# Performance work log

Measured on AMD Instinct MI355X. Metric: run time of the kernel, lower is better.

## Reference

```python
import jax, jax.numpy as jnp
import numpy as np

IN_SIZE = 1024
CLASSES = 7
N = 50000
LN_EPS = 1e-5


def _chain(x, w, b, g, beta):
    # Linear -> (Dropout=identity at eval) -> LayerNorm -> GELU(exact erf)
    h = x @ w.T + b
    mu = jnp.mean(h, axis=-1, keepdims=True)
    var = jnp.var(h, axis=-1, keepdims=True)
    h = (h - mu) / jnp.sqrt(var + LN_EPS) * g + beta
    return jax.nn.gelu(h, approximate=False)


def setup_inputs() -> dict:
    key = jax.random.key(0)
    ks = jax.random.split(key, 16)
    d = IN_SIZE
    std = 1.0 / np.sqrt(d)
    inp = {
        "features": jax.random.normal(ks[0], (N, d), jnp.float32),
        "c": jax.random.normal(ks[1], (N, CLASSES), jnp.float32),
        "key_w": jax.random.uniform(ks[2], (d, d), jnp.float32, -std, std),
        "key_b": jax.random.uniform(ks[3], (d,), jnp.float32, -std, std),
        "key_g": jnp.ones((d,), jnp.float32),
        "key_beta": jnp.zeros((d,), jnp.float32),
        "query_w": jax.random.uniform(ks[4], (d, d), jnp.float32, -std, std),
        "query_b": jax.random.uniform(ks[5], (d,), jnp.float32, -std, std),
        "query_g": jnp.ones((d,), jnp.float32),
        "query_beta": jnp.zeros((d,), jnp.float32),
        "value_w": jax.random.uniform(ks[6], (d, d), jnp.float32, -std, std),
        "value_b": jax.random.uniform(ks[7], (d,), jnp.float32, -std, std),
        "value_g": jnp.ones((d,), jnp.float32),
        "value_beta": jnp.zeros((d,), jnp.float32),
        "head_w": jax.random.uniform(ks[8], (CLASSES, CLASSES, d), jnp.float32, -1.0 / np.sqrt(CLASSES * d), 1.0 / np.sqrt(CLASSES * d)),
        "head_b": jax.random.uniform(ks[9], (CLASSES,), jnp.float32, -1.0 / np.sqrt(CLASSES * d), 1.0 / np.sqrt(CLASSES * d)),
    }
    return inp


def reference(features, c, key_w, key_b, key_g, key_beta,
              query_w, query_b, query_g, query_beta,
              value_w, value_b, value_g, value_beta,
              head_w, head_b):
    K = _chain(features, key_w, key_b, key_g, key_beta)          # [N, d]
    V = _chain(K, value_w, value_b, value_g, value_beta)         # [N, d]
    Q = _chain(K, query_w, query_b, query_g, query_beta)         # [N, d]
    # critical (top-scoring) instance per class
    top_idx = jnp.argmax(c, axis=0)                              # [classes]
    m_feats = K[top_idx]                                         # [classes, d]
    q_max = _chain(m_feats, query_w, query_b, query_g, query_beta)  # [classes, d]
    A = Q @ q_max.T                                              # [N, classes]
    A = jax.nn.softmax(A / jnp.sqrt(jnp.float32(Q.shape[1])), axis=0)
    B = A.T @ V                                                  # [classes, d]
    # Conv1d(classes, classes, kernel_size=d) on [1, classes, d] -> full contraction
    C = jnp.einsum('ik,oik->o', B, head_w) + head_b              # [classes]
    C = C.reshape(1, -1)
    return (C, A, B.reshape(1, CLASSES, -1))
```

## Files before the change

### kernel.cpp

```cpp
#include <hip/hip_runtime.h>


typedef unsigned short u16;
typedef __attribute__((ext_vector_type(8))) short          bf16x8;
typedef __attribute__((ext_vector_type(8))) unsigned short u16x8;
typedef __attribute__((ext_vector_type(4))) unsigned short u16x4;
typedef __attribute__((ext_vector_type(4))) float          f32x4;

#define DDIM  1024
#define NROWS 50000
#define MP    50176
#define NCLS  7
#define MPD4  12544

__device__ __forceinline__ u16 f2bf(float f) {
  unsigned u = __float_as_uint(f);
  u = (u + 0x7FFFu + ((u >> 16) & 1u)) >> 16;
  return (u16)u;
}
__device__ __forceinline__ float bf2f(u16 h) {
  return __uint_as_float(((unsigned)h) << 16);
}
__device__ __forceinline__ float gelu(float x) {
  return 0.5f * x * (1.0f + erff(x * 0.70710678118654752f));
}

__device__ __forceinline__ void load16_lds(const u16* g, u16* l) {
  __builtin_amdgcn_global_load_lds(
      (const __attribute__((address_space(1))) unsigned int*)(const void*)g,
      (__attribute__((address_space(3))) unsigned int*)(void*)l, 16, 0, 0);
}

#define MFMA_(a, b, c) __builtin_amdgcn_mfma_f32_16x16x32_bf16(a, b, c, 0, 0, 0)

__global__ __launch_bounds__(256) void k_convert(const float* __restrict__ src,
                                                 u16* __restrict__ dst,
                                                 int rows_total, int rows_valid) {
  const size_t total = (size_t)rows_total * DDIM / 8;
  const size_t stride = (size_t)gridDim.x * blockDim.x;
  for (size_t i = (size_t)blockIdx.x * blockDim.x + threadIdx.x; i < total; i += stride) {
    const size_t e = i * 8;
    const int row = (int)(e >> 10);
    u16x8 o = {0, 0, 0, 0, 0, 0, 0, 0};
    if (row < rows_valid) {
      const float4* p = (const float4*)(src + e);
      float4 f0 = p[0], f1 = p[1];
      o[0] = f2bf(f0.x); o[1] = f2bf(f0.y); o[2] = f2bf(f0.z); o[3] = f2bf(f0.w);
      o[4] = f2bf(f1.x); o[5] = f2bf(f1.y); o[6] = f2bf(f1.z); o[7] = f2bf(f1.w);
    }
    *(u16x8*)(dst + e) = o;
  }
}

__global__ __launch_bounds__(256) void k_convw(const float* __restrict__ kw,
                                               const float* __restrict__ vw,
                                               const float* __restrict__ qw,
                                               u16* __restrict__ Wk,
                                               u16* __restrict__ Wvq) {
  const int w = blockIdx.x >> 7;
  const int b = blockIdx.x & 127;
  const float* src = (w == 0) ? kw : (w == 1) ? vw : qw;
  u16* dst = (w == 0) ? Wk : (Wvq + (size_t)(w - 1) * DDIM * DDIM);
  for (int i = b * 256 + threadIdx.x; i < DDIM * DDIM / 8; i += 128 * 256) {
    const float4* p = (const float4*)(src + (size_t)i * 8);
    float4 f0 = p[0], f1 = p[1];
    u16x8 o;
    o[0] = f2bf(f0.x); o[1] = f2bf(f0.y); o[2] = f2bf(f0.z); o[3] = f2bf(f0.w);
    o[4] = f2bf(f1.x); o[5] = f2bf(f1.y); o[6] = f2bf(f1.z); o[7] = f2bf(f1.w);
    *(u16x8*)(dst + (size_t)i * 8) = o;
  }
}

__global__ __launch_bounds__(512, 2) void k_gemm256(const u16* __restrict__ A,
                                                    const u16* __restrict__ Bw,
                                                    u16* __restrict__ C,
                                                    int lnn, int ldc) {
  extern __shared__ __align__(16) u16 smem[];
  u16* Abase = smem;
  u16* Bbase = smem + 49152;
  const int tid  = threadIdx.x;
  const int lane = tid & 63;
  const int wid  = tid >> 6;
  const int wr = wid >> 2;
  const int wc = wid & 3;
  const int bh = wc >> 1;
  const int bl = (wc & 1) * 64;
  const int fr = lane & 15;
  const int T  = lane >> 4;
  const int cpx = gridDim.x >> 3;
  const int v  = (blockIdx.x & 7) * cpx + (blockIdx.x >> 3);
  const int m0 = (v >> lnn) * 256;
  const int n0 = (v & ((1 << lnn) - 1)) * 256;

  f32x4 acc[8][4] = {};

#define STAGE_A(KT, BB) do {                                                   \
    _Pragma("unroll") for (int h_ = 0; h_ < 2; ++h_)                           \
      _Pragma("unroll") for (int l_ = 0; l_ < 2; ++l_) {                       \
        const int s_ = l_ * 512 + tid;                                         \
        const int r_ = s_ >> 3;                                                \
        const int c_ = (s_ & 7) ^ (r_ & 7);                                    \
        load16_lds(A + (size_t)(m0 + h_ * 128 + r_) * DDIM + (KT) * 64 + c_ * 8, \
                   Abase + (BB) * 16384 + h_ * 8192 + s_ * 8);                 \
      } } while (0)

#define STAGE_B(KT) do {                                                       \
    _Pragma("unroll") for (int h_ = 0; h_ < 2; ++h_)                           \
      _Pragma("unroll") for (int l_ = 0; l_ < 2; ++l_) {                       \
        const int s_ = l_ * 512 + tid;                                         \
        const int r_ = s_ >> 3;                                                \
        const int c_ = (s_ & 7) ^ (r_ & 7);                                    \
        load16_lds(Bw + (size_t)(n0 + h_ * 128 + r_) * DDIM + (KT) * 64 + c_ * 8, \
                   Bbase + h_ * 8192 + s_ * 8);                                \
      } } while (0)

#define PHASE_A(p) do {                                                        \
    bf16x8 afr[4];                                                             \
    _Pragma("unroll") for (int ks = 0; ks < 2; ++ks)                           \
      _Pragma("unroll") for (int ii = 0; ii < 2; ++ii) {                       \
        const int R = ((p) * 2 + ii) * 16 + fr;                                \
        afr[ks * 2 + ii] = *(const bf16x8*)&Ap[R * 64 + (((ks * 4 + T) ^ (R & 7)) << 3)]; \
      }                                                                        \
    __builtin_amdgcn_s_setprio(1);                                             \
    _Pragma("unroll") for (int ks = 0; ks < 2; ++ks)                           \
      _Pragma("unroll") for (int ii = 0; ii < 2; ++ii)                         \
        _Pragma("unroll") for (int j = 0; j < 4; ++j)                          \
          acc[(p) * 2 + ii][j] = MFMA_(afr[ks * 2 + ii], bfr[ks * 4 + j],      \
                                       acc[(p) * 2 + ii][j]);                  \
    __builtin_amdgcn_s_setprio(0);                                             \
  } while (0)

#define BARP() asm volatile("s_barrier" ::: "memory")

  STAGE_A(0, 0);
  STAGE_B(0);
  STAGE_A(1, 1);
  asm volatile("s_waitcnt vmcnt(4)\n\ts_barrier" ::: "memory");

  for (int kt = 0; kt < 16; ++kt) {
    const u16* Ap = Abase + (kt % 3) * 16384 + wr * 8192;
    const u16* Bp = Bbase + bh * 8192;
    bf16x8 bfr[8];
#pragma unroll
    for (int ks = 0; ks < 2; ++ks)
#pragma unroll
      for (int j = 0; j < 4; ++j) {
        const int R = bl + j * 16 + fr;
        bfr[ks * 4 + j] = *(const bf16x8*)&Bp[R * 64 + (((ks * 4 + T) ^ (R & 7)) << 3)];
      }
    PHASE_A(0);
    BARP();
    if (kt < 15) STAGE_B(kt + 1);
    PHASE_A(1);
    BARP();
    if (kt < 14) STAGE_A(kt + 2, (kt + 2) % 3);
    PHASE_A(2);
    BARP();
    PHASE_A(3);
    if (kt < 14)
      asm volatile("s_waitcnt vmcnt(4)\n\ts_barrier" ::: "memory");
    else if (kt == 14)
      asm volatile("s_waitcnt vmcnt(0)\n\ts_barrier" ::: "memory");
  }
#undef STAGE_A
#undef STAGE_B
#undef PHASE_A
#undef BARP

#pragma unroll
  for (int i = 0; i < 8; ++i)
#pragma unroll
    for (int j = 0; j < 4; ++j) {
      const size_t base = (size_t)(m0 + wr * 128 + i * 16 + T * 4) * ldc
                        + (n0 + wc * 64 + j * 16 + fr);
#pragma unroll
      for (int r = 0; r < 4; ++r)
        C[base + (size_t)r * ldc] = f2bf(acc[i][j][r]);
    }
}

__global__ __launch_bounds__(256) void k_ln_k(const u16* __restrict__ h,
                                              const float* __restrict__ bias,
                                              const float* __restrict__ g,
                                              const float* __restrict__ beta,
                                              u16* __restrict__ out) {
  const int lane = threadIdx.x & 63;
  const int row = blockIdx.x * 4 + (threadIdx.x >> 6);
  const int c0 = lane * 8;
  u16x8* op0 = (u16x8*)(out + (size_t)row * DDIM + c0);
  u16x8* op1 = (u16x8*)(out + (size_t)row * DDIM + 512 + c0);
  if (row >= NROWS) {
    u16x8 z = {0, 0, 0, 0, 0, 0, 0, 0};
    *op0 = z; *op1 = z;
    return;
  }
  u16x8 h0 = *(const u16x8*)(h + (size_t)row * DDIM + c0);
  u16x8 h1 = *(const u16x8*)(h + (size_t)row * DDIM + 512 + c0);
  float4 a0 = *(const float4*)(bias + c0), a1 = *(const float4*)(bias + c0 + 4);
  float4 a2 = *(const float4*)(bias + 512 + c0), a3 = *(const float4*)(bias + 512 + c0 + 4);
  const float ba[8] = {a0.x, a0.y, a0.z, a0.w, a1.x, a1.y, a1.z, a1.w};
  const float bb[8] = {a2.x, a2.y, a2.z, a2.w, a3.x, a3.y, a3.z, a3.w};
  float v0[8], v1[8];
  float s1 = 0.f, s2 = 0.f;
#pragma unroll
  for (int e = 0; e < 8; ++e) {
    v0[e] = bf2f(h0[e]) + ba[e];
    v1[e] = bf2f(h1[e]) + bb[e];
    s1 += v0[e] + v1[e];
    s2 += v0[e] * v0[e] + v1[e] * v1[e];
  }
#pragma unroll
  for (int m = 1; m < 64; m <<= 1) {
    s1 += __shfl_xor(s1, m, 64);
    s2 += __shfl_xor(s2, m, 64);
  }
  const float mu = s1 * (1.0f / 1024.0f);
  const float var = s2 * (1.0f / 1024.0f) - mu * mu;
  const float rs = rsqrtf(var + 1e-5f);
  float4 g0 = *(const float4*)(g + c0), g1 = *(const float4*)(g + c0 + 4);
  float4 g2 = *(const float4*)(g + 512 + c0), g3 = *(const float4*)(g + 512 + c0 + 4);
  float4 t0 = *(const float4*)(beta + c0), t1 = *(const float4*)(beta + c0 + 4);
  float4 t2 = *(const float4*)(beta + 512 + c0), t3 = *(const float4*)(beta + 512 + c0 + 4);
  const float ga[8] = {g0.x, g0.y, g0.z, g0.w, g1.x, g1.y, g1.z, g1.w};
  const float gb[8] = {g2.x, g2.y, g2.z, g2.w, g3.x, g3.y, g3.z, g3.w};
  const float ta[8] = {t0.x, t0.y, t0.z, t0.w, t1.x, t1.y, t1.z, t1.w};
  const float tb[8] = {t2.x, t2.y, t2.z, t2.w, t3.x, t3.y, t3.z, t3.w};
  u16x8 o0, o1;
#pragma unroll
  for (int e = 0; e < 8; ++e) {
    o0[e] = f2bf(gelu((v0[e] - mu) * rs * ga[e] + ta[e]));
    o1[e] = f2bf(gelu((v1[e] - mu) * rs * gb[e] + tb[e]));
  }
  *op0 = o0; *op1 = o1;
}

__global__ __launch_bounds__(64) void k_qmax2(const float* __restrict__ argv,
                                              const int* __restrict__ argi,
                                              const u16* __restrict__ hvq,
                                              const float* __restrict__ qb,
                                              const float* __restrict__ qg,
                                              const float* __restrict__ qbeta,
                                              u16* __restrict__ qm) {
  const int j = blockIdx.x;
  const int lane = threadIdx.x;
  float bv = -3.4e38f; int bi = 0x7fffffff;
  for (int p = lane; p < 128; p += 64) {
    const float v = argv[p * NCLS + j];
    const int   i = argi[p * NCLS + j];
    if (v > bv || (v == bv && i < bi)) { bv = v; bi = i; }
  }
#pragma unroll
  for (int m = 1; m < 64; m <<= 1) {
    const float ov = __shfl_xor(bv, m, 64);
    const int   oi = __shfl_xor(bi, m, 64);
    if (ov > bv || (ov == bv && oi < bi)) { bv = ov; bi = oi; }
  }
  const int row = bi;
  const int c0 = lane * 8;
  const u16* hp = hvq + (size_t)row * 2048 + DDIM;
  u16x8 h0 = *(const u16x8*)(hp + c0);
  u16x8 h1 = *(const u16x8*)(hp + 512 + c0);
  float v0[8], v1[8];
  float s1 = 0.f, s2 = 0.f;
#pragma unroll
  for (int e = 0; e < 8; ++e) {
    v0[e] = bf2f(h0[e]) + qb[c0 + e];
    v1[e] = bf2f(h1[e]) + qb[512 + c0 + e];
    s1 += v0[e] + v1[e];
    s2 += v0[e] * v0[e] + v1[e] * v1[e];
  }
#pragma unroll
  for (int m = 1; m < 64; m <<= 1) {
    s1 += __shfl_xor(s1, m, 64);
    s2 += __shfl_xor(s2, m, 64);
  }
  const float mu = s1 * (1.0f / 1024.0f);
  const float var = s2 * (1.0f / 1024.0f) - mu * mu;
  const float rs = rsqrtf(var + 1e-5f);
  u16x8 o0, o1;
#pragma unroll
  for (int e = 0; e < 8; ++e) {
    o0[e] = f2bf(gelu((v0[e] - mu) * rs * qg[c0 + e] + qbeta[c0 + e]));
    o1[e] = f2bf(gelu((v1[e] - mu) * rs * qg[512 + c0 + e] + qbeta[512 + c0 + e]));
  }
  *(u16x8*)(qm + (size_t)j * DDIM + c0) = o0;
  *(u16x8*)(qm + (size_t)j * DDIM + 512 + c0) = o1;
}

__global__ __launch_bounds__(256) void k_ln_vq(const u16* __restrict__ h,
                                               const float* __restrict__ v_b,
                                               const float* __restrict__ v_g,
                                               const float* __restrict__ v_beta,
                                               const float* __restrict__ q_b,
                                               const float* __restrict__ q_g,
                                               const float* __restrict__ q_beta,
                                               const u16* __restrict__ qm,
                                               u16* __restrict__ V,
                                               float* __restrict__ logits) {
  __shared__ __align__(16) u16 sqm[NCLS * DDIM];
  const int tid = threadIdx.x;
  const int lane = tid & 63;
  const int half = (blockIdx.x >= MPD4) ? 1 : 0;
  const int rb = half ? (blockIdx.x - MPD4) : blockIdx.x;
  const int row = rb * 4 + (tid >> 6);
  if (half) {
    for (int i = tid; i < NCLS * DDIM / 8; i += 256)
      *(u16x8*)&sqm[i * 8] = *(const u16x8*)&qm[i * 8];
    __syncthreads();
  }
  if (row >= NROWS) return;
  const float* bias = half ? q_b : v_b;
  const float* gain = half ? q_g : v_g;
  const float* bet  = half ? q_beta : v_beta;
  const int c0 = lane * 8;
  const u16* hp = h + (size_t)row * 2048 + (size_t)half * DDIM;
  u16x8 h0 = *(const u16x8*)(hp + c0);
  u16x8 h1 = *(const u16x8*)(hp + 512 + c0);
  float4 a0 = *(const float4*)(bias + c0), a1 = *(const float4*)(bias + c0 + 4);
  float4 a2 = *(const float4*)(bias + 512 + c0), a3 = *(const float4*)(bias + 512 + c0 + 4);
  const float ba[8] = {a0.x, a0.y, a0.z, a0.w, a1.x, a1.y, a1.z, a1.w};
  const float bb[8] = {a2.x, a2.y, a2.z, a2.w, a3.x, a3.y, a3.z, a3.w};
  float v0[8], v1[8];
  float s1 = 0.f, s2 = 0.f;
#pragma unroll
  for (int e = 0; e < 8; ++e) {
    v0[e] = bf2f(h0[e]) + ba[e];
    v1[e] = bf2f(h1[e]) + bb[e];
    s1 += v0[e] + v1[e];
    s2 += v0[e] * v0[e] + v1[e] * v1[e];
  }
#pragma unroll
  for (int m = 1; m < 64; m <<= 1) {
    s1 += __shfl_xor(s1, m, 64);
    s2 += __shfl_xor(s2, m, 64);
  }
  const float mu = s1 * (1.0f / 1024.0f);
  const float var = s2 * (1.0f / 1024.0f) - mu * mu;
  const float rs = rsqrtf(var + 1e-5f);
  float4 g0 = *(const float4*)(gain + c0), g1 = *(const float4*)(gain + c0 + 4);
  float4 g2 = *(const float4*)(gain + 512 + c0), g3 = *(const float4*)(gain + 512 + c0 + 4);
  float4 t0 = *(const float4*)(bet + c0), t1 = *(const float4*)(bet + c0 + 4);
  float4 t2 = *(const float4*)(bet + 512 + c0), t3 = *(const float4*)(bet + 512 + c0 + 4);
  const float ga[8] = {g0.x, g0.y, g0.z, g0.w, g1.x, g1.y, g1.z, g1.w};
  const float gb[8] = {g2.x, g2.y, g2.z, g2.w, g3.x, g3.y, g3.z, g3.w};
  const float ta[8] = {t0.x, t0.y, t0.z, t0.w, t1.x, t1.y, t1.z, t1.w};
  const float tb[8] = {t2.x, t2.y, t2.z, t2.w, t3.x, t3.y, t3.z, t3.w};
  float y0[8], y1[8];
#pragma unroll
  for (int e = 0; e < 8; ++e) {
    y0[e] = gelu((v0[e] - mu) * rs * ga[e] + ta[e]);
    y1[e] = gelu((v1[e] - mu) * rs * gb[e] + tb[e]);
  }
  if (half == 0) {
    u16x8 o0, o1;
#pragma unroll
    for (int e = 0; e < 8; ++e) { o0[e] = f2bf(y0[e]); o1[e] = f2bf(y1[e]); }
    *(u16x8*)(V + (size_t)row * DDIM + c0) = o0;
    *(u16x8*)(V + (size_t)row * DDIM + 512 + c0) = o1;
  } else {
#pragma unroll
    for (int j = 0; j < NCLS; ++j) {
      u16x8 m0 = *(const u16x8*)&sqm[j * DDIM + c0];
      u16x8 m1 = *(const u16x8*)&sqm[j * DDIM + 512 + c0];
      float p = 0.f;
#pragma unroll
      for (int e = 0; e < 8; ++e) p += y0[e] * bf2f(m0[e]) + y1[e] * bf2f(m1[e]);
#pragma unroll
      for (int m = 1; m < 64; m <<= 1) p += __shfl_xor(p, m, 64);
      if (lane == 0) logits[(size_t)row * NCLS + j] = p * 0.03125f;
    }
  }
}

__global__ __launch_bounds__(256) void k_arg1(const float* __restrict__ c,
                                              float* __restrict__ pv,
                                              int* __restrict__ pi) {
  __shared__ float sv[256 * NCLS];
  __shared__ int   si[256 * NCLS];
  const int t = threadIdx.x;
  float bv[NCLS]; int bi[NCLS];
#pragma unroll
  for (int j = 0; j < NCLS; ++j) { bv[j] = -3.4e38f; bi[j] = 0x7fffffff; }
  for (int n = blockIdx.x * 256 + t; n < NROWS; n += 128 * 256) {
#pragma unroll
    for (int j = 0; j < NCLS; ++j) {
      const float v = c[(size_t)n * NCLS + j];
      if (v > bv[j]) { bv[j] = v; bi[j] = n; }
    }
  }
#pragma unroll
  for (int j = 0; j < NCLS; ++j) { sv[t * NCLS + j] = bv[j]; si[t * NCLS + j] = bi[j]; }
  __syncthreads();
  for (int s = 128; s > 0; s >>= 1) {
    if (t < s) {
#pragma unroll
      for (int j = 0; j < NCLS; ++j) {
        const float v2 = sv[(t + s) * NCLS + j]; const int i2 = si[(t + s) * NCLS + j];
        const float v1 = sv[t * NCLS + j];       const int i1 = si[t * NCLS + j];
        if (v2 > v1 || (v2 == v1 && i2 < i1)) { sv[t * NCLS + j] = v2; si[t * NCLS + j] = i2; }
      }
    }
    __syncthreads();
  }
  if (t < NCLS) { pv[blockIdx.x * NCLS + t] = sv[t]; pi[blockIdx.x * NCLS + t] = si[t]; }
}

__global__ __launch_bounds__(256) void k_softpart(const float* __restrict__ logits,
                                                  float* __restrict__ Pm,
                                                  float* __restrict__ Ps) {
  __shared__ float sm[256 * NCLS];
  const int t = threadIdx.x;
  float m[NCLS];
#pragma unroll
  for (int j = 0; j < NCLS; ++j) m[j] = -3.4e38f;
  for (int n = blockIdx.x * 256 + t; n < NROWS; n += 128 * 256)
#pragma unroll
    for (int j = 0; j < NCLS; ++j) m[j] = fmaxf(m[j], logits[(size_t)n * NCLS + j]);
#pragma unroll
  for (int j = 0; j < NCLS; ++j) sm[t * NCLS + j] = m[j];
  __syncthreads();
  for (int s = 128; s > 0; s >>= 1) {
    if (t < s)
#pragma unroll
      for (int j = 0; j < NCLS; ++j)
        sm[t * NCLS + j] = fmaxf(sm[t * NCLS + j], sm[(t + s) * NCLS + j]);
    __syncthreads();
  }
  float mloc[NCLS];
#pragma unroll
  for (int j = 0; j < NCLS; ++j) mloc[j] = sm[j];
  __syncthreads();
  float s[NCLS];
#pragma unroll
  for (int j = 0; j < NCLS; ++j) s[j] = 0.f;
  for (int n = blockIdx.x * 256 + t; n < NROWS; n += 128 * 256)
#pragma unroll
    for (int j = 0; j < NCLS; ++j) s[j] += expf(logits[(size_t)n * NCLS + j] - mloc[j]);
#pragma unroll
  for (int j = 0; j < NCLS; ++j) sm[t * NCLS + j] = s[j];
  __syncthreads();
  for (int st = 128; st > 0; st >>= 1) {
    if (t < st)
#pragma unroll
      for (int j = 0; j < NCLS; ++j) sm[t * NCLS + j] += sm[(t + st) * NCLS + j];
    __syncthreads();
  }
  if (t < NCLS) { Pm[blockIdx.x * NCLS + t] = mloc[t]; Ps[blockIdx.x * NCLS + t] = sm[t]; }
}

__global__ __launch_bounds__(256) void k_bpart(const float* __restrict__ logits,
                                               const float* __restrict__ Pm,
                                               const float* __restrict__ Ps,
                                               const u16* __restrict__ V,
                                               float* __restrict__ Aout,
                                               float* __restrict__ Pb) {
  __shared__ float sA[98 * NCLS];
  __shared__ float sM[NCLS], sR[NCLS];
  const int t = threadIdx.x;
  if (t < NCLS) {
    float M = -3.4e38f;
    for (int b = 0; b < 128; ++b) M = fmaxf(M, Pm[b * NCLS + t]);
    float S = 0.f;
    for (int b = 0; b < 128; ++b) S += Ps[b * NCLS + t] * expf(Pm[b * NCLS + t] - M);
    sM[t] = M; sR[t] = 1.0f / S;
  }
  __syncthreads();
  const int n0 = blockIdx.x * 98;
  int cnt = NROWS - n0;
  cnt = cnt < 0 ? 0 : (cnt > 98 ? 98 : cnt);
  for (int idx = t; idx < cnt * NCLS; idx += 256) {
    const int j = idx % NCLS;
    const float a = expf(logits[(size_t)n0 * NCLS + idx] - sM[j]) * sR[j];
    sA[idx] = a;
    Aout[(size_t)n0 * NCLS + idx] = a;
  }
  __syncthreads();
  float acc[NCLS][4] = {};
  for (int r = 0; r < cnt; ++r) {
    u16x4 vv = *(const u16x4*)&V[(size_t)(n0 + r) * DDIM + t * 4];
    const float f0 = bf2f(vv[0]), f1 = bf2f(vv[1]), f2 = bf2f(vv[2]), f3 = bf2f(vv[3]);
#pragma unroll
    for (int j = 0; j < NCLS; ++j) {
      const float a = sA[r * NCLS + j];
      acc[j][0] += a * f0; acc[j][1] += a * f1; acc[j][2] += a * f2; acc[j][3] += a * f3;
    }
  }
#pragma unroll
  for (int j = 0; j < NCLS; ++j) {
    f32x4 o = {acc[j][0], acc[j][1], acc[j][2], acc[j][3]};
    *(f32x4*)&Pb[((size_t)blockIdx.x * NCLS + j) * DDIM + t * 4] = o;
  }
}

__global__ void k_bred(const float* __restrict__ Pb, float* __restrict__ Bout) {
  const int idx = blockIdx.x * 256 + threadIdx.x;
  if (idx >= NCLS * DDIM) return;
  float s = 0.f;
  for (int p = 0; p < 512; ++p) s += Pb[(size_t)p * NCLS * DDIM + idx];
  Bout[idx] = s;
}

__global__ __launch_bounds__(256) void k_head(const float* __restrict__ Bmat,
                                              const float* __restrict__ hw,
                                              const float* __restrict__ hb,
                                              float* __restrict__ Cout) {
  const int o = blockIdx.x, t = threadIdx.x;
  float p = 0.f;
  for (int idx = t; idx < NCLS * DDIM; idx += 256)
    p += Bmat[idx] * hw[(size_t)o * NCLS * DDIM + idx];
#pragma unroll
  for (int m = 1; m < 64; m <<= 1) p += __shfl_xor(p, m, 64);
  __shared__ float w[4];
  if ((t & 63) == 0) w[t >> 6] = p;
  __syncthreads();
  if (t == 0) Cout[o] = w[0] + w[1] + w[2] + w[3] + hb[o];
}

extern "C" void kernel_launch(void* const* d_in, const int* in_sizes, int n_in,
                              void* d_out, int out_size, void* d_ws, size_t ws_size,
                              hipStream_t stream) {
  const float* features   = (const float*)d_in[0];
  const float* c_in       = (const float*)d_in[1];
  const float* key_w      = (const float*)d_in[2];
  const float* key_b      = (const float*)d_in[3];
  const float* key_g      = (const float*)d_in[4];
  const float* key_beta   = (const float*)d_in[5];
  const float* query_w    = (const float*)d_in[6];
  const float* query_b    = (const float*)d_in[7];
  const float* query_g    = (const float*)d_in[8];
  const float* query_beta = (const float*)d_in[9];
  const float* value_w    = (const float*)d_in[10];
  const float* value_b    = (const float*)d_in[11];
  const float* value_g    = (const float*)d_in[12];
  const float* value_beta = (const float*)d_in[13];
  const float* head_w     = (const float*)d_in[14];
  const float* head_b     = (const float*)d_in[15];

  char* ws = (char*)d_ws;
  const size_t SZB = (size_t)MP * DDIM * 2;
  u16* Xb   = (u16*)ws;
  u16* HbK  = (u16*)(ws + SZB);
  u16* HbVQ = Xb;
  u16* Kb   = (u16*)(ws + 2 * SZB);
  u16* Vb   = Kb;
  size_t off = 3 * SZB;
  u16* Wk  = (u16*)(ws + off); off += (size_t)DDIM * DDIM * 2;
  u16* Wvq = (u16*)(ws + off); off += (size_t)2 * DDIM * DDIM * 2;
  float* logits = (float*)(ws + off); off += ((size_t)NROWS * NCLS * 4 + 255) & ~(size_t)255;
  float* Pb  = (float*)(ws + off); off += (size_t)512 * NCLS * DDIM * 4;
  u16* qm    = (u16*)(ws + off); off += ((size_t)NCLS * DDIM * 2 + 255) & ~(size_t)255;
  float* Pmax = (float*)(ws + off); off += ((size_t)128 * NCLS * 4 + 255) & ~(size_t)255;
  float* Psum = (float*)(ws + off); off += ((size_t)128 * NCLS * 4 + 255) & ~(size_t)255;
  float* argv = (float*)(ws + off); off += ((size_t)128 * NCLS * 4 + 255) & ~(size_t)255;
  int*   argi = (int*)  (ws + off); off += ((size_t)128 * NCLS * 4 + 255) & ~(size_t)255;

  float* Cout = (float*)d_out;
  float* Aout = Cout + NCLS;
  float* Bout = Aout + (size_t)NROWS * NCLS;

  k_arg1<<<128, 256, 0, stream>>>(c_in, argv, argi);
  k_convw<<<384, 256, 0, stream>>>(key_w, value_w, query_w, Wk, Wvq);
  k_convert<<<2048, 256, 0, stream>>>(features, Xb, MP, NROWS);

  k_gemm256<<<784, 512, 131072, stream>>>(Xb, Wk, HbK, 2, 1024);
  k_ln_k<<<MPD4, 256, 0, stream>>>(HbK, key_b, key_g, key_beta, Kb);

  k_gemm256<<<1568, 512, 131072, stream>>>(Kb, Wvq, HbVQ, 3, 2048);
  k_qmax2<<<NCLS, 64, 0, stream>>>(argv, argi, HbVQ, query_b, query_g, query_beta, qm);
  k_ln_vq<<<2 * MPD4, 256, 0, stream>>>(HbVQ, value_b, value_g, value_beta,
                                        query_b, query_g, query_beta, qm, Vb, logits);

  k_softpart<<<128, 256, 0, stream>>>(logits, Pmax, Psum);

  k_bpart<<<512, 256, 0, stream>>>(logits, Pmax, Psum, Vb, Aout, Pb);
  k_bred<<<28, 256, 0, stream>>>(Pb, Bout);
  k_head<<<NCLS, 256, 0, stream>>>(Bout, head_w, head_b, Cout);
}
```

Before: 667.0 us.

## Restructure GEMM main loop into ping-pong phases with split B fragment reads

Reorganizes the inner k-loop of the bf16 MFMA GEMM into four phases that each read A/B fragments from LDS and then issue 16 MFMAs, separated by workgroup barriers. Global-to-LDS staging of the next B and A tiles is moved between phases, so waves alternate memory and compute work. The goal is better overlap of LDS reads and global loads with MFMA execution. The cost is more barriers per iteration, which can stall if the waves fall out of balance.

```diff
diff --git a/kernel.cpp b/kernel.cpp
--- a/kernel.cpp
+++ b/kernel.cpp
@@ -94,77 +94,84 @@
 
   f32x4 acc[8][4] = {};
 
-#define STAGE_A(KT, BB) do {                                                   \
-    _Pragma("unroll") for (int h_ = 0; h_ < 2; ++h_)                           \
-      _Pragma("unroll") for (int l_ = 0; l_ < 2; ++l_) {                       \
-        const int s_ = l_ * 512 + tid;                                         \
-        const int r_ = s_ >> 3;                                                \
-        const int c_ = (s_ & 7) ^ (r_ & 7);                                    \
-        load16_lds(A + (size_t)(m0 + h_ * 128 + r_) * DDIM + (KT) * 64 + c_ * 8, \
-                   Abase + (BB) * 16384 + h_ * 8192 + s_ * 8);                 \
-      } } while (0)
-
-#define STAGE_B(KT) do {                                                       \
-    _Pragma("unroll") for (int h_ = 0; h_ < 2; ++h_)                           \
-      _Pragma("unroll") for (int l_ = 0; l_ < 2; ++l_) {                       \
-        const int s_ = l_ * 512 + tid;                                         \
-        const int r_ = s_ >> 3;                                                \
-        const int c_ = (s_ & 7) ^ (r_ & 7);                                    \
-        load16_lds(Bw + (size_t)(n0 + h_ * 128 + r_) * DDIM + (KT) * 64 + c_ * 8, \
-                   Bbase + h_ * 8192 + s_ * 8);                                \
-      } } while (0)
-
-#define PHASE_A(p) do {                                                        \
-    bf16x8 afr[4];                                                             \
-    _Pragma("unroll") for (int ks = 0; ks < 2; ++ks)                           \
-      _Pragma("unroll") for (int ii = 0; ii < 2; ++ii) {                       \
-        const int R = ((p) * 2 + ii) * 16 + fr;                                \
-        afr[ks * 2 + ii] = *(const bf16x8*)&Ap[R * 64 + (((ks * 4 + T) ^ (R & 7)) << 3)]; \
-      }                                                                        \
+#define STAGE_AH(KT, HH) do {                                                  \
+    _Pragma("unroll") for (int l_ = 0; l_ < 2; ++l_) {                         \
+      const int s_ = l_ * 512 + tid;                                           \
+      const int r_ = s_ >> 3;                                                  \
+      const int c_ = (s_ & 7) ^ (r_ & 7);                                      \
+      load16_lds(A + (size_t)(m0 + (HH) * 128 + r_) * DDIM + (KT) * 64 + c_ * 8, \
+                 Abase + ((KT) % 3) * 16384 + (HH) * 8192 + s_ * 8);           \
+    } } while (0)
+
+#define STAGE_BH(KT, HH) do {                                                  \
+    _Pragma("unroll") for (int l_ = 0; l_ < 2; ++l_) {                         \
+      const int s_ = l_ * 512 + tid;                                           \
+      const int r_ = s_ >> 3;                                                  \
+      const int c_ = (s_ & 7) ^ (r_ & 7);                                      \
+      load16_lds(Bw + (size_t)(n0 + (HH) * 128 + r_) * DDIM + (KT) * 64 + c_ * 8, \
+                 Bbase + (HH) * 8192 + s_ * 8);                                \
+    } } while (0)
+
+#define READ_B(DST, KS) do {                                                   \
+    _Pragma("unroll") for (int j_ = 0; j_ < 4; ++j_) {                         \
+      const int R = bl + j_ * 16 + fr;                                         \
+      DST[j_] = *(const bf16x8*)&Bp[R * 64 + ((((KS) * 4 + T) ^ (R & 7)) << 3)]; \
+    } } while (0)
+
+#define READ_A(RH, KS) do {                                                    \
+    _Pragma("unroll") for (int r_ = 0; r_ < 4; ++r_) {                         \
+      const int R = ((RH) * 4 + r_) * 16 + fr;                                 \
+      af[r_] = *(const bf16x8*)&Ap[R * 64 + ((((KS) * 4 + T) ^ (R & 7)) << 3)]; \
+    } } while (0)
+
+#define MFMA16(RH, BF) do {                                                    \
     __builtin_amdgcn_s_setprio(1);                                             \
-    _Pragma("unroll") for (int ks = 0; ks < 2; ++ks)                           \
-      _Pragma("unroll") for (int ii = 0; ii < 2; ++ii)                         \
-        _Pragma("unroll") for (int j = 0; j < 4; ++j)                          \
-          acc[(p) * 2 + ii][j] = MFMA_(afr[ks * 2 + ii], bfr[ks * 4 + j],      \
-                                       acc[(p) * 2 + ii][j]);                  \
+    _Pragma("unroll") for (int r_ = 0; r_ < 4; ++r_)                           \
+      _Pragma("unroll") for (int j_ = 0; j_ < 4; ++j_)                         \
+        acc[(RH) * 4 + r_][j_] = MFMA_(af[r_], BF[j_], acc[(RH) * 4 + r_][j_]); \
     __builtin_amdgcn_s_setprio(0);                                             \
   } while (0)
 
 #define BARP() asm volatile("s_barrier" ::: "memory")
 
-  STAGE_A(0, 0);
-  STAGE_B(0);
-  STAGE_A(1, 1);
+  STAGE_AH(0, 0); STAGE_AH(0, 1);
+  STAGE_BH(0, 0); STAGE_BH(0, 1);
+  STAGE_AH(1, 0); STAGE_AH(1, 1);
   asm volatile("s_waitcnt vmcnt(4)\n\ts_barrier" ::: "memory");
 
   for (int kt = 0; kt < 16; ++kt) {
     const u16* Ap = Abase + (kt % 3) * 16384 + wr * 8192;
     const u16* Bp = Bbase + bh * 8192;
-    bf16x8 bfr[8];
-#pragma unroll
-    for (int ks = 0; ks < 2; ++ks)
-#pragma unroll
-      for (int j = 0; j < 4; ++j) {
-        const int R = bl + j * 16 + fr;
-        bfr[ks * 4 + j] = *(const bf16x8*)&Bp[R * 64 + (((ks * 4 + T) ^ (R & 7)) << 3)];
-      }
-    PHASE_A(0);
-    BARP();
-    if (kt < 15) STAGE_B(kt + 1);
-    PHASE_A(1);
-    BARP();
-    if (kt < 14) STAGE_A(kt + 2, (kt + 2) % 3);
-    PHASE_A(2);
-    BARP();
-    PHASE_A(3);
+    bf16x8 b0[4], b1[4], af[4];
+    READ_B(b0, 0);
+    READ_A(0, 0);
+    BARP();
+    MFMA16(0, b0);
+    BARP();
+    READ_B(b1, 1);
+    READ_A(0, 1);
+    BARP();
+    MFMA16(0, b1);
+    BARP();
+    READ_A(1, 0);
+    if (kt < 15) { STAGE_BH(kt + 1, 0); STAGE_BH(kt + 1, 1); }
+    BARP();
+    MFMA16(1, b0);
+    BARP();
+    READ_A(1, 1);
+    if (kt < 14) { STAGE_AH(kt + 2, 0); STAGE_AH(kt + 2, 1); }
+    BARP();
+    MFMA16(1, b1);
     if (kt < 14)
       asm volatile("s_waitcnt vmcnt(4)\n\ts_barrier" ::: "memory");
     else if (kt == 14)
       asm volatile("s_waitcnt vmcnt(0)\n\ts_barrier" ::: "memory");
   }
-#undef STAGE_A
-#undef STAGE_B
-#undef PHASE_A
+#undef STAGE_AH
+#undef STAGE_BH
+#undef READ_A
+#undef READ_B
+#undef MFMA16
 #undef BARP
 
 #pragma unroll
```

Measured after the change: 677.4 us. About the same (+1.6%).

## Fuse value LayerNorm+GELU into attention-weighted B partial reduction

Applied to the files above, without the earlier changes.

The value-branch LayerNorm+GELU moves out of the combined LN kernel and into the B partial-sum kernel. That kernel now reads the raw value GEMM output, normalizes each row per wave, computes the softmax weights and accumulates A^T·V in registers. The partial sums from the four waves are merged through shared memory. This removes the bf16 V write and re-read over 50k×1024 elements. In exchange, the transcendental-heavy GELU work runs on only 512 blocks with large per-thread accumulators (7×16 floats), which risks register pressure and low occupancy.

```diff
diff --git a/kernel.cpp b/kernel.cpp
--- a/kernel.cpp
+++ b/kernel.cpp
@@ -287,37 +287,26 @@
   *(u16x8*)(qm + (size_t)j * DDIM + 512 + c0) = o1;
 }
 
-__global__ __launch_bounds__(256) void k_ln_vq(const u16* __restrict__ h,
-                                               const float* __restrict__ v_b,
-                                               const float* __restrict__ v_g,
-                                               const float* __restrict__ v_beta,
-                                               const float* __restrict__ q_b,
-                                               const float* __restrict__ q_g,
-                                               const float* __restrict__ q_beta,
-                                               const u16* __restrict__ qm,
-                                               u16* __restrict__ V,
-                                               float* __restrict__ logits) {
+__global__ __launch_bounds__(256) void k_ln_q(const u16* __restrict__ h,
+                                              const float* __restrict__ q_b,
+                                              const float* __restrict__ q_g,
+                                              const float* __restrict__ q_beta,
+                                              const u16* __restrict__ qm,
+                                              float* __restrict__ logits) {
   __shared__ __align__(16) u16 sqm[NCLS * DDIM];
   const int tid = threadIdx.x;
   const int lane = tid & 63;
-  const int half = (blockIdx.x >= MPD4) ? 1 : 0;
-  const int rb = half ? (blockIdx.x - MPD4) : blockIdx.x;
-  const int row = rb * 4 + (tid >> 6);
-  if (half) {
-    for (int i = tid; i < NCLS * DDIM / 8; i += 256)
-      *(u16x8*)&sqm[i * 8] = *(const u16x8*)&qm[i * 8];
-    __syncthreads();
-  }
+  const int row = blockIdx.x * 4 + (tid >> 6);
+  for (int i = tid; i < NCLS * DDIM / 8; i += 256)
+    *(u16x8*)&sqm[i * 8] = *(const u16x8*)&qm[i * 8];
+  __syncthreads();
   if (row >= NROWS) return;
-  const float* bias = half ? q_b : v_b;
-  const float* gain = half ? q_g : v_g;
-  const float* bet  = half ? q_beta : v_beta;
   const int c0 = lane * 8;
-  const u16* hp = h + (size_t)row * 2048 + (size_t)half * DDIM;
+  const u16* hp = h + (size_t)row * 2048 + DDIM;
   u16x8 h0 = *(const u16x8*)(hp + c0);
   u16x8 h1 = *(const u16x8*)(hp + 512 + c0);
-  float4 a0 = *(const float4*)(bias + c0), a1 = *(const float4*)(bias + c0 + 4);
-  float4 a2 = *(const float4*)(bias + 512 + c0), a3 = *(const float4*)(bias + 512 + c0 + 4);
+  float4 a0 = *(const float4*)(q_b + c0), a1 = *(const float4*)(q_b + c0 + 4);
+  float4 a2 = *(const float4*)(q_b + 512 + c0), a3 = *(const float4*)(q_b + 512 + c0 + 4);
   const float ba[8] = {a0.x, a0.y, a0.z, a0.w, a1.x, a1.y, a1.z, a1.w};
   const float bb[8] = {a2.x, a2.y, a2.z, a2.w, a3.x, a3.y, a3.z, a3.w};
   float v0[8], v1[8];
@@ -337,10 +326,10 @@
   const float mu = s1 * (1.0f / 1024.0f);
   const float var = s2 * (1.0f / 1024.0f) - mu * mu;
   const float rs = rsqrtf(var + 1e-5f);
-  float4 g0 = *(const float4*)(gain + c0), g1 = *(const float4*)(gain + c0 + 4);
-  float4 g2 = *(const float4*)(gain + 512 + c0), g3 = *(const float4*)(gain + 512 + c0 + 4);
-  float4 t0 = *(const float4*)(bet + c0), t1 = *(const float4*)(bet + c0 + 4);
-  float4 t2 = *(const float4*)(bet + 512 + c0), t3 = *(const float4*)(bet + 512 + c0 + 4);
+  float4 g0 = *(const float4*)(q_g + c0), g1 = *(const float4*)(q_g + c0 + 4);
+  float4 g2 = *(const float4*)(q_g + 512 + c0), g3 = *(const float4*)(q_g + 512 + c0 + 4);
+  float4 t0 = *(const float4*)(q_beta + c0), t1 = *(const float4*)(q_beta + c0 + 4);
+  float4 t2 = *(const float4*)(q_beta + 512 + c0), t3 = *(const float4*)(q_beta + 512 + c0 + 4);
   const float ga[8] = {g0.x, g0.y, g0.z, g0.w, g1.x, g1.y, g1.z, g1.w};
   const float gb[8] = {g2.x, g2.y, g2.z, g2.w, g3.x, g3.y, g3.z, g3.w};
   const float ta[8] = {t0.x, t0.y, t0.z, t0.w, t1.x, t1.y, t1.z, t1.w};
@@ -351,24 +340,16 @@
     y0[e] = gelu((v0[e] - mu) * rs * ga[e] + ta[e]);
     y1[e] = gelu((v1[e] - mu) * rs * gb[e] + tb[e]);
   }
-  if (half == 0) {
-    u16x8 o0, o1;
-#pragma unroll
-    for (int e = 0; e < 8; ++e) { o0[e] = f2bf(y0[e]); o1[e] = f2bf(y1[e]); }
-    *(u16x8*)(V + (size_t)row * DDIM + c0) = o0;
-    *(u16x8*)(V + (size_t)row * DDIM + 512 + c0) = o1;
-  } else {
-#pragma unroll
-    for (int j = 0; j < NCLS; ++j) {
-      u16x8 m0 = *(const u16x8*)&sqm[j * DDIM + c0];
-      u16x8 m1 = *(const u16x8*)&sqm[j * DDIM + 512 + c0];
-      float p = 0.f;
-#pragma unroll
-      for (int e = 0; e < 8; ++e) p += y0[e] * bf2f(m0[e]) + y1[e] * bf2f(m1[e]);
-#pragma unroll
-      for (int m = 1; m < 64; m <<= 1) p += __shfl_xor(p, m, 64);
-      if (lane == 0) logits[(size_t)row * NCLS + j] = p * 0.03125f;
-    }
+#pragma unroll
+  for (int j = 0; j < NCLS; ++j) {
+    u16x8 m0 = *(const u16x8*)&sqm[j * DDIM + c0];
+    u16x8 m1 = *(const u16x8*)&sqm[j * DDIM + 512 + c0];
+    float p = 0.f;
+#pragma unroll
+    for (int e = 0; e < 8; ++e) p += y0[e] * bf2f(m0[e]) + y1[e] * bf2f(m1[e]);
+#pragma unroll
+    for (int m = 1; m < 64; m <<= 1) p += __shfl_xor(p, m, 64);
+    if (lane == 0) logits[(size_t)row * NCLS + j] = p * 0.03125f;
   }
 }
 
@@ -448,15 +429,20 @@
   if (t < NCLS) { Pm[blockIdx.x * NCLS + t] = mloc[t]; Ps[blockIdx.x * NCLS + t] = sm[t]; }
 }
 
-__global__ __launch_bounds__(256) void k_bpart(const float* __restrict__ logits,
-                                               const float* __restrict__ Pm,
-                                               const float* __restrict__ Ps,
-                                               const u16* __restrict__ V,
-                                               float* __restrict__ Aout,
-                                               float* __restrict__ Pb) {
-  __shared__ float sA[98 * NCLS];
+__global__ __launch_bounds__(256) void k_bpartv(const float* __restrict__ logits,
+                                                const float* __restrict__ Pm,
+                                                const float* __restrict__ Ps,
+                                                const u16* __restrict__ hvq,
+                                                const float* __restrict__ v_b,
+                                                const float* __restrict__ v_g,
+                                                const float* __restrict__ v_beta,
+                                                float* __restrict__ Aout,
+                                                float* __restrict__ Pb) {
   __shared__ float sM[NCLS], sR[NCLS];
+  __shared__ float smerge[NCLS * DDIM];
   const int t = threadIdx.x;
+  const int lane = t & 63;
+  const int w = t >> 6;
   if (t < NCLS) {
     float M = -3.4e38f;
     for (int b = 0; b < 128; ++b) M = fmaxf(M, Pm[b * NCLS + t]);
@@ -464,32 +450,81 @@
     for (int b = 0; b < 128; ++b) S += Ps[b * NCLS + t] * expf(Pm[b * NCLS + t] - M);
     sM[t] = M; sR[t] = 1.0f / S;
   }
+  for (int i = t; i < NCLS * DDIM; i += 256) smerge[i] = 0.f;
   __syncthreads();
+
+  const int c0 = lane * 16;
+  float4 b0 = *(const float4*)(v_b + c0),    b1 = *(const float4*)(v_b + c0 + 4);
+  float4 b2 = *(const float4*)(v_b + c0 + 8), b3 = *(const float4*)(v_b + c0 + 12);
+  const float bb[16] = {b0.x,b0.y,b0.z,b0.w, b1.x,b1.y,b1.z,b1.w,
+                        b2.x,b2.y,b2.z,b2.w, b3.x,b3.y,b3.z,b3.w};
+  float4 g0 = *(const float4*)(v_g + c0),    g1 = *(const float4*)(v_g + c0 + 4);
+  float4 g2 = *(const float4*)(v_g + c0 + 8), g3 = *(const float4*)(v_g + c0 + 12);
+  const float gg[16] = {g0.x,g0.y,g0.z,g0.w, g1.x,g1.y,g1.z,g1.w,
+                        g2.x,g2.y,g2.z,g2.w, g3.x,g3.y,g3.z,g3.w};
+  float4 t0 = *(const float4*)(v_beta + c0),    t1 = *(const float4*)(v_beta + c0 + 4);
+  float4 t2 = *(const float4*)(v_beta + c0 + 8), t3 = *(const float4*)(v_beta + c0 + 12);
+  const float tt[16] = {t0.x,t0.y,t0.z,t0.w, t1.x,t1.y,t1.z,t1.w,
+                        t2.x,t2.y,t2.z,t2.w, t3.x,t3.y,t3.z,t3.w};
+
   const int n0 = blockIdx.x * 98;
   int cnt = NROWS - n0;
   cnt = cnt < 0 ? 0 : (cnt > 98 ? 98 : cnt);
-  for (int idx = t; idx < cnt * NCLS; idx += 256) {
-    const int j = idx % NCLS;
-    const float a = expf(logits[(size_t)n0 * NCLS + idx] - sM[j]) * sR[j];
-    sA[idx] = a;
-    Aout[(size_t)n0 * NCLS + idx] = a;
-  }
-  __syncthreads();
-  float acc[NCLS][4] = {};
-  for (int r = 0; r < cnt; ++r) {
-    u16x4 vv = *(const u16x4*)&V[(size_t)(n0 + r) * DDIM + t * 4];
-    const float f0 = bf2f(vv[0]), f1 = bf2f(vv[1]), f2 = bf2f(vv[2]), f3 = bf2f(vv[3]);
-#pragma unroll
-    for (int j = 0; j < NCLS; ++j) {
-      const float a = sA[r * NCLS + j];
-      acc[j][0] += a * f0; acc[j][1] += a * f1; acc[j][2] += a * f2; acc[j][3] += a * f3;
-    }
-  }
-#pragma unroll
-  for (int j = 0; j < NCLS; ++j) {
-    f32x4 o = {acc[j][0], acc[j][1], acc[j][2], acc[j][3]};
-    *(f32x4*)&Pb[((size_t)blockIdx.x * NCLS + j) * DDIM + t * 4] = o;
-  }
+
+  float acc[NCLS][16] = {};
+  for (int r = w; r < cnt; r += 4) {
+    const int n = n0 + r;
+    const u16* hp = hvq + (size_t)n * 2048 + c0;
+    u16x8 h0 = *(const u16x8*)hp;
+    u16x8 h1 = *(const u16x8*)(hp + 8);
+    float vv[16];
+    float s1 = 0.f, s2 = 0.f;
+#pragma unroll
+    for (int e = 0; e < 8; ++e) {
+      vv[e]     = bf2f(h0[e]) + bb[e];
+      vv[e + 8] = bf2f(h1[e]) + bb[e + 8];
+    }
+#pragma unroll
+    for (int e = 0; e < 16; ++e) { s1 += vv[e]; s2 += vv[e] * vv[e]; }
+#pragma unroll
+    for (int m = 1; m < 64; m <<= 1) {
+      s1 += __shfl_xor(s1, m, 64);
+      s2 += __shfl_xor(s2, m, 64);
+    }
+    const float mu = s1 * (1.0f / 1024.0f);
+    const float var = s2 * (1.0f / 1024.0f) - mu * mu;
+    const float rs = rsqrtf(var + 1e-5f);
+    float y[16];
+#pragma unroll
+    for (int e = 0; e < 16; ++e)
+      y[e] = gelu((vv[e] - mu) * rs * gg[e] + tt[e]);
+    float a[NCLS];
+#pragma unroll
+    for (int j = 0; j < NCLS; ++j)
+      a[j] = expf(logits[(size_t)n * NCLS + j] - sM[j]) * sR[j];
+    if (lane < NCLS) {
+      const float av = expf(logits[(size_t)n * NCLS + lane] - sM[lane]) * sR[lane];
+      Aout[(size_t)n * NCLS + lane] = av;
+    }
+#pragma unroll
+    for (int j = 0; j < NCLS; ++j)
+#pragma unroll
+      for (int e = 0; e < 16; ++e)
+        acc[j][e] += a[j] * y[e];
+  }
+
+  for (int ww = 0; ww < 4; ++ww) {
+    if (w == ww) {
+#pragma unroll
+      for (int j = 0; j < NCLS; ++j)
+#pragma unroll
+        for (int e = 0; e < 16; ++e)
+          smerge[j * DDIM + c0 + e] += acc[j][e];
+    }
+    __syncthreads();
+  }
+  for (int i = t; i < NCLS * DDIM; i += 256)
+    Pb[(size_t)blockIdx.x * NCLS * DDIM + i] = smerge[i];
 }
 
 __global__ void k_bred(const float* __restrict__ Pb, float* __restrict__ Bout) {
@@ -542,7 +577,6 @@
   u16* HbK  = (u16*)(ws + SZB);
   u16* HbVQ = Xb;
   u16* Kb   = (u16*)(ws + 2 * SZB);
-  u16* Vb   = Kb;
   size_t off = 3 * SZB;
   u16* Wk  = (u16*)(ws + off); off += (size_t)DDIM * DDIM * 2;
   u16* Wvq = (u16*)(ws + off); off += (size_t)2 * DDIM * DDIM * 2;
@@ -567,12 +601,12 @@
 
   k_gemm256<<<1568, 512, 131072, stream>>>(Kb, Wvq, HbVQ, 3, 2048);
   k_qmax2<<<NCLS, 64, 0, stream>>>(argv, argi, HbVQ, query_b, query_g, query_beta, qm);
-  k_ln_vq<<<2 * MPD4, 256, 0, stream>>>(HbVQ, value_b, value_g, value_beta,
-                                        query_b, query_g, query_beta, qm, Vb, logits);
+  k_ln_q<<<MPD4, 256, 0, stream>>>(HbVQ, query_b, query_g, query_beta, qm, logits);
 
   k_softpart<<<128, 256, 0, stream>>>(logits, Pmax, Psum);
 
-  k_bpart<<<512, 256, 0, stream>>>(logits, Pmax, Psum, Vb, Aout, Pb);
+  k_bpartv<<<512, 256, 0, stream>>>(logits, Pmax, Psum, HbVQ,
+                                    value_b, value_g, value_beta, Aout, Pb);
   k_bred<<<28, 256, 0, stream>>>(Pb, Bout);
   k_head<<<NCLS, 256, 0, stream>>>(Bout, head_w, head_b, Cout);
 }
```

Result: slower. 767.4 us (+15.0%).
